# Optimization experiments

Measured on AMD Instinct MI355X. Metric: run time of the kernel, lower is better.

Reference implementation:

```python
import jax, jax.numpy as jnp
import numpy as np

B, T, D, H, FA = 512, 64, 128, 128, 64


def setup_inputs() -> dict:
    key = jax.random.key(0)
    ks = jax.random.split(key, 14)
    n = lambda k, s: jax.random.normal(k, s, dtype=jnp.float32) * 0.05
    return {
        "X": jax.random.normal(ks[0], (B, T, D), dtype=jnp.float32),
        "attri_data": jax.random.normal(ks[1], (D, FA), dtype=jnp.float32),
        "w_attr1": n(ks[2], (FA, FA // 2)), "b_attr1": n(ks[3], (FA // 2,)),
        "w_attr2": n(ks[4], (FA // 2, 1)), "b_attr2": n(ks[5], (1,)),
        "w_a1": n(ks[6], (2 * H + T, H)), "b_a1": n(ks[7], (H,)),
        "w_a2": n(ks[8], (H, 1)), "b_a2": n(ks[9], (1,)),
        "w_ih": n(ks[10], (4 * H, D)), "w_hh": n(ks[11], (4 * H, H)),
        "b_ih": n(ks[12], (4 * H,)), "b_hh": n(ks[13], (4 * H,)),
    }


def reference(X, attri_data, w_attr1, b_attr1, w_attr2, b_attr2,
              w_a1, b_a1, w_a2, b_a2, w_ih, w_hh, b_ih, b_hh):
    b, t_dim, d = X.shape
    h_dim = w_hh.shape[1]

    # Attribute attention: softmax over the data_dim axis (dim=0)
    a = attri_data @ w_attr1 + b_attr1
    a = jnp.where(a > 0, a, 0.5 * a)  # LeakyReLU(negative_slope=0.5)
    alpha_attri = jax.nn.softmax(a @ w_attr2 + b_attr2, axis=0)  # [D, 1]
    X_attri = X * alpha_attri.reshape(1, 1, d)  # [B, T, D]
    Xp = jnp.transpose(X_attri, (0, 2, 1))      # [B, D, T] per-variable series

    def step(carry, x_t):  # x_t: [B, D]
        h, c = carry  # [B, H] each; state BEFORE consuming x_t (matches torch loop)
        feat = jnp.concatenate([
            jnp.broadcast_to(h[:, None, :], (b, d, h_dim)),
            jnp.broadcast_to(c[:, None, :], (b, d, h_dim)),
            Xp,
        ], axis=2)  # [B, D, 2H+T]
        e = jnp.tanh(feat @ w_a1 + b_a1) @ w_a2 + b_a2  # [B, D, 1]
        alpha_s = jax.nn.softmax(e[..., 0], axis=1)      # softmax over D
        x_tilde_t = alpha_s * x_t                        # [B, D]
        # LSTM cell (PyTorch gate order i, f, g, o)
        gates = x_t @ w_ih.T + b_ih + h @ w_hh.T + b_hh  # [B, 4H]
        i_g, f_g, g_g, o_g = jnp.split(gates, 4, axis=1)
        c_new = jax.nn.sigmoid(f_g) * c + jax.nn.sigmoid(i_g) * jnp.tanh(g_g)
        h_new = jax.nn.sigmoid(o_g) * jnp.tanh(c_new)
        return (h_new, c_new), x_tilde_t

    h0 = jnp.zeros((b, h_dim), X.dtype)
    c0 = jnp.zeros((b, h_dim), X.dtype)
    _, X_tilde = jax.lax.scan(step, (h0, c0), jnp.transpose(X_attri, (1, 0, 2)))
    return jnp.transpose(X_tilde, (1, 0, 2))  # [B, T, D]
```

## Files before the change

### kernel.cpp

```cpp
#include <hip/hip_runtime.h>
#include <hip/hip_bf16.h>
#include <cstddef>
#include <cstdint>

#define DEVI __device__ __forceinline__

typedef float f32x4 __attribute__((ext_vector_type(4)));
typedef __bf16 bf16x8 __attribute__((ext_vector_type(8)));

DEVI float fast_rcp(float x) { return __builtin_amdgcn_rcpf(x); }
DEVI float sigmoid_fast(float x) { return fast_rcp(1.0f + __expf(-x)); }
DEVI float tanh_fast(float x) { return 1.0f - 2.0f * fast_rcp(__expf(2.0f * x) + 1.0f); }
DEVI float4 ld4(const float* p) { return *reinterpret_cast<const float4*>(p); }
DEVI void st4(float* p, float4 v) { *reinterpret_cast<float4*>(p) = v; }
DEVI float f4c(const float4& v, int i) { return i == 0 ? v.x : i == 1 ? v.y : i == 2 ? v.z : v.w; }
DEVI unsigned short bfbits(float f) { return __builtin_bit_cast(unsigned short, (__bf16)f); }
DEVI unsigned pack2(float a, float b) {
  return (unsigned)bfbits(a) | ((unsigned)bfbits(b) << 16);
}

__global__ __launch_bounds__(128) void k_alpha(
    const float* __restrict__ AD, const float* __restrict__ W1,
    const float* __restrict__ B1, const float* __restrict__ W2,
    const float* __restrict__ B2, float* __restrict__ alpha) {
  __shared__ float sW1[64 * 32];
  __shared__ float sW2[32];
  __shared__ float sB1[32];
  __shared__ float red[128];
  __shared__ float s_mx, s_sum;
  int tid = threadIdx.x;
  for (int i = tid; i < 64 * 32; i += 128) sW1[i] = W1[i];
  if (tid < 32) { sW2[tid] = W2[tid]; sB1[tid] = B1[tid]; }
  __syncthreads();
  float ad[64];
  #pragma unroll
  for (int f = 0; f < 64; ++f) ad[f] = AD[tid * 64 + f];
  float logit = B2[0];
  #pragma unroll
  for (int j = 0; j < 32; ++j) {
    float a = sB1[j];
    #pragma unroll
    for (int f = 0; f < 64; ++f) a = fmaf(ad[f], sW1[f * 32 + j], a);
    a = a > 0.0f ? a : 0.5f * a;
    logit = fmaf(a, sW2[j], logit);
  }
  red[tid] = logit;
  __syncthreads();
  if (tid == 0) {
    float mx = red[0];
    for (int i = 1; i < 128; ++i) mx = fmaxf(mx, red[i]);
    float sm = 0.0f;
    for (int i = 0; i < 128; ++i) sm += __expf(red[i] - mx);
    s_mx = mx; s_sum = sm;
  }
  __syncthreads();
  alpha[tid] = __expf(logit - s_mx) / s_sum;
}

__global__ __launch_bounds__(256) void k_ep(
    const float* __restrict__ X, const float* __restrict__ w_a1,
    const float* __restrict__ b_a1, const float* __restrict__ alpha,
    float* __restrict__ EP) {
  __shared__ float Xb[64][128];
  __shared__ float Wx[64][128];
  int b = blockIdx.x;
  int tid = threadIdx.x;
  #pragma unroll
  for (int i = 0; i < 8; ++i) {
    int l4 = i * 256 + tid;
    int r = l4 >> 5, c4 = l4 & 31;
    st4(&Xb[r][c4 * 4], ld4(&X[((size_t)b * 64 + r) * 128 + c4 * 4]));
    st4(&Wx[r][c4 * 4], ld4(&w_a1[(size_t)(256 + r) * 128 + c4 * 4]));
  }
  __syncthreads();
  int dg = tid & 15, kg = tid >> 4;
  float acc[8][8] = {};
  #pragma unroll 4
  for (int tau = 0; tau < 64; ++tau) {
    float4 xa0 = ld4(&Xb[tau][dg * 4]);
    float4 xa1 = ld4(&Xb[tau][64 + dg * 4]);
    float4 wa0 = ld4(&Wx[tau][kg * 4]);
    float4 wa1 = ld4(&Wx[tau][64 + kg * 4]);
    #pragma unroll
    for (int i = 0; i < 8; ++i) {
      float xv = (i < 4) ? f4c(xa0, i) : f4c(xa1, i - 4);
      #pragma unroll
      for (int j = 0; j < 4; ++j) {
        acc[i][j]     = fmaf(xv, f4c(wa0, j), acc[i][j]);
        acc[i][j + 4] = fmaf(xv, f4c(wa1, j), acc[i][j + 4]);
      }
    }
  }
  float4 ba0 = ld4(&b_a1[kg * 4]);
  float4 ba1v = ld4(&b_a1[64 + kg * 4]);
  #pragma unroll
  for (int i = 0; i < 8; ++i) {
    int drow = (i < 4) ? dg * 4 + i : 64 + dg * 4 + (i - 4);
    float al = alpha[drow];
    float4 o0, o1;
    float* p0 = &o0.x; float* p1 = &o1.x;
    #pragma unroll
    for (int j = 0; j < 4; ++j) {
      float v0 = 2.0f * fmaf(al, acc[i][j],     f4c(ba0, j));
      float v1 = 2.0f * fmaf(al, acc[i][j + 4], f4c(ba1v, j));
      p0[j] = __expf(fminf(fmaxf(v0, -40.0f), 40.0f));
      p1[j] = __expf(fminf(fmaxf(v1, -40.0f), 40.0f));
    }
    st4(&EP[((size_t)b * 128 + drow) * 128 + kg * 4], o0);
    st4(&EP[((size_t)b * 128 + drow) * 128 + 64 + kg * 4], o1);
  }
}

__global__ __launch_bounds__(512, 2) void k_rec(
    const float* __restrict__ X, const float* __restrict__ w_ih,
    const float* __restrict__ w_hh, const float* __restrict__ b_ih,
    const float* __restrict__ b_hh, const float* __restrict__ alpha,
    float* __restrict__ S) {
  __shared__ unsigned short kB[16 * 256];
  int tid = threadIdx.x;
  int wv = tid >> 6, l = tid & 63, lg = l >> 4, lr = l & 15;
  int b0 = blockIdx.x * 16;

  bf16x8 afr[8][4];
  #pragma unroll
  for (int ks = 0; ks < 8; ++ks) {
    int kb = (ks & 3) * 32 + lg * 8;
    float4 a0, a1;
    if (ks < 4) { a0 = ld4(&alpha[kb]); a1 = ld4(&alpha[kb + 4]); }
    #pragma unroll
    for (int q = 0; q < 4; ++q) {
      int j = q * 128 + wv * 16 + lr;
      const float* src = (ks < 4) ? &w_ih[(size_t)j * 128 + kb]
                                  : &w_hh[(size_t)j * 128 + kb];
      float4 f0 = ld4(src), f1 = ld4(src + 4);
      if (ks < 4) {
        f0.x *= a0.x; f0.y *= a0.y; f0.z *= a0.z; f0.w *= a0.w;
        f1.x *= a1.x; f1.y *= a1.y; f1.z *= a1.z; f1.w *= a1.w;
      }
      bf16x8 fr;
      fr[0] = (__bf16)f0.x; fr[1] = (__bf16)f0.y;
      fr[2] = (__bf16)f0.z; fr[3] = (__bf16)f0.w;
      fr[4] = (__bf16)f1.x; fr[5] = (__bf16)f1.y;
      fr[6] = (__bf16)f1.z; fr[7] = (__bf16)f1.w;
      afr[ks][q] = fr;
    }
  }

  float bias[4][4];
  #pragma unroll
  for (int q = 0; q < 4; ++q)
    #pragma unroll
    for (int r = 0; r < 4; ++r) {
      int j = q * 128 + wv * 16 + lg * 4 + r;
      bias[q][r] = b_ih[j] + b_hh[j];
    }

  alignas(16) float hA[4] = {0.f, 0.f, 0.f, 0.f};
  alignas(16) float cA[4] = {0.f, 0.f, 0.f, 0.f};

  int bi = tid >> 5, d4 = tid & 31, d0 = d4 * 4;
  int m0 = wv * 16 + lg * 4;
  int k0 = 128 + m0;
  unsigned short* xdst = &kB[bi * 256 + (((d0 >> 3) ^ (bi & 7)) << 3) + (d0 & 7)];
  unsigned short* hdst = &kB[lr * 256 + ((((k0 >> 3) ^ (lr & 7))) << 3) + (k0 & 7)];

  for (int t = 0; t < 64; ++t) {
    size_t srow = ((size_t)(t * 512) + b0 + lr) * 256;
    st4(&S[srow + m0], *reinterpret_cast<const float4*>(hA));
    st4(&S[srow + 128 + m0], *reinterpret_cast<const float4*>(cA));

    float4 xv = ld4(&X[(((size_t)(b0 + bi)) * 64 + t) * 128 + d0]);
    uint2 xu; xu.x = pack2(xv.x, xv.y); xu.y = pack2(xv.z, xv.w);
    *reinterpret_cast<uint2*>(xdst) = xu;

    uint2 hu; hu.x = pack2(hA[0], hA[1]); hu.y = pack2(hA[2], hA[3]);
    *reinterpret_cast<uint2*>(hdst) = hu;

    __syncthreads();

    bf16x8 bfr[8];
    #pragma unroll
    for (int ks = 0; ks < 8; ++ks) {
      int kb = ks * 32 + lg * 8;
      int idx = lr * 256 + (((kb >> 3) ^ (lr & 7)) << 3) + (kb & 7);
      bfr[ks] = *reinterpret_cast<const bf16x8*>(&kB[idx]);
    }

    f32x4 acc0 = {0.f, 0.f, 0.f, 0.f}, acc1 = acc0, acc2 = acc0, acc3 = acc0;
    #pragma unroll
    for (int ks = 0; ks < 8; ++ks) {
      acc0 = __builtin_amdgcn_mfma_f32_16x16x32_bf16(afr[ks][0], bfr[ks], acc0, 0, 0, 0);
      acc1 = __builtin_amdgcn_mfma_f32_16x16x32_bf16(afr[ks][1], bfr[ks], acc1, 0, 0, 0);
      acc2 = __builtin_amdgcn_mfma_f32_16x16x32_bf16(afr[ks][2], bfr[ks], acc2, 0, 0, 0);
      acc3 = __builtin_amdgcn_mfma_f32_16x16x32_bf16(afr[ks][3], bfr[ks], acc3, 0, 0, 0);
    }

    #pragma unroll
    for (int r = 0; r < 4; ++r) {
      float ig = sigmoid_fast(acc0[r] + bias[0][r]);
      float fg = sigmoid_fast(acc1[r] + bias[1][r]);
      float gg = tanh_fast(acc2[r] + bias[2][r]);
      float og = sigmoid_fast(acc3[r] + bias[3][r]);
      float cn = fmaf(fg, cA[r], ig * gg);
      float hn = og * tanh_fast(cn);
      cA[r] = cn;
      hA[r] = hn;
    }
    __syncthreads();
  }
}

__global__ __launch_bounds__(256) void k_eq(
    const float* __restrict__ S, const float* __restrict__ w_a1,
    float* __restrict__ EQ) {
  __shared__ float Ss[64][68];
  __shared__ float Wc[64][128];
  int r0 = blockIdx.x * 64;
  int tid = threadIdx.x;
  int kg = tid & 15, rg = tid >> 4;
  int rr = rg * 4;
  float acc[4][8] = {};
  for (int kc = 0; kc < 4; ++kc) {
    if (kc) __syncthreads();
    #pragma unroll
    for (int i = 0; i < 4; ++i) {
      int l4 = i * 256 + tid;
      int r = l4 >> 4, c4 = l4 & 15;
      st4(&Ss[r][c4 * 4], ld4(&S[(size_t)(r0 + r) * 256 + kc * 64 + c4 * 4]));
    }
    #pragma unroll
    for (int i = 0; i < 8; ++i) {
      int l4 = i * 256 + tid;
      int r = l4 >> 5, c4 = l4 & 31;
      st4(&Wc[r][c4 * 4], ld4(&w_a1[(size_t)(kc * 64 + r) * 128 + c4 * 4]));
    }
    __syncthreads();
    #pragma unroll 2
    for (int k = 0; k < 64; k += 4) {
      float4 sa[4];
      #pragma unroll
      for (int i = 0; i < 4; ++i) sa[i] = ld4(&Ss[rr + i][k]);
      #pragma unroll
      for (int kk = 0; kk < 4; ++kk) {
        float4 wa0 = ld4(&Wc[k + kk][kg * 4]);
        float4 wa1 = ld4(&Wc[k + kk][64 + kg * 4]);
        #pragma unroll
        for (int i = 0; i < 4; ++i) {
          float sv = f4c(sa[i], kk);
          #pragma unroll
          for (int j = 0; j < 4; ++j) {
            acc[i][j]     = fmaf(sv, f4c(wa0, j), acc[i][j]);
            acc[i][j + 4] = fmaf(sv, f4c(wa1, j), acc[i][j + 4]);
          }
        }
      }
    }
  }
  #pragma unroll
  for (int i = 0; i < 4; ++i) {
    float4 o0, o1;
    float* p0 = &o0.x; float* p1 = &o1.x;
    #pragma unroll
    for (int j = 0; j < 4; ++j) {
      float v0 = 2.0f * acc[i][j];
      float v1 = 2.0f * acc[i][j + 4];
      p0[j] = __expf(fminf(fmaxf(v0, -40.0f), 40.0f));
      p1[j] = __expf(fminf(fmaxf(v1, -40.0f), 40.0f));
    }
    st4(&EQ[(size_t)(r0 + rr + i) * 128 + kg * 4], o0);
    st4(&EQ[(size_t)(r0 + rr + i) * 128 + 64 + kg * 4], o1);
  }
}

__global__ __launch_bounds__(512, 4) void k_attn(
    const float* __restrict__ EP, const float* __restrict__ EQ,
    const float* __restrict__ w_a2, const float* __restrict__ alpha,
    const float* __restrict__ X, float* __restrict__ out) {
  __shared__ float EQs[64][128];
  __shared__ float e_lds[128];
  int b = blockIdx.x;
  int tid = threadIdx.x;
  #pragma unroll
  for (int i = 0; i < 4; ++i) {
    int l4 = i * 512 + tid;
    int t = l4 >> 5, k4 = l4 & 31;
    st4(&EQs[t][k4 * 4], ld4(&EQ[((size_t)t * 512 + b) * 128 + k4 * 4]));
  }
  int d = tid >> 2, s = tid & 3;
  float4 ep[8], w2r[8];
  #pragma unroll
  for (int q = 0; q < 8; ++q) {
    ep[q]  = ld4(&EP[((size_t)b * 128 + d) * 128 + s * 32 + q * 4]);
    w2r[q] = ld4(&w_a2[s * 32 + q * 4]);
  }
  __syncthreads();
  for (int t = 0; t < 64; ++t) {
    float p = 0.0f;
    #pragma unroll
    for (int q = 0; q < 8; ++q) {
      float4 eq = ld4(&EQs[t][s * 32 + q * 4]);
      p = fmaf(w2r[q].x, fast_rcp(fmaf(ep[q].x, eq.x, 1.0f)), p);
      p = fmaf(w2r[q].y, fast_rcp(fmaf(ep[q].y, eq.y, 1.0f)), p);
      p = fmaf(w2r[q].z, fast_rcp(fmaf(ep[q].z, eq.z, 1.0f)), p);
      p = fmaf(w2r[q].w, fast_rcp(fmaf(ep[q].w, eq.w, 1.0f)), p);
    }
    p += __shfl_xor(p, 1);
    p += __shfl_xor(p, 2);
    if (s == 0) e_lds[d] = -2.0f * p;
    __syncthreads();
    if (tid < 128) {
      int lane = tid & 63;
      float v0 = e_lds[lane], v1 = e_lds[64 + lane];
      float mx = fmaxf(v0, v1);
      #pragma unroll
      for (int o = 1; o < 64; o <<= 1) mx = fmaxf(mx, __shfl_xor(mx, o));
      float e0 = __expf(v0 - mx), e1 = __expf(v1 - mx);
      float sm = e0 + e1;
      #pragma unroll
      for (int o = 1; o < 64; o <<= 1) sm += __shfl_xor(sm, o);
      float inv = fast_rcp(sm);
      float ev = (tid < 64) ? e0 : e1;
      float av = ev * inv * alpha[tid];
      out[((size_t)b * 64 + t) * 128 + tid] = av * X[((size_t)b * 64 + t) * 128 + tid];
    }
    __syncthreads();
  }
}

extern "C" void kernel_launch(void* const* d_in, const int* in_sizes, int n_in,
                              void* d_out, int out_size, void* d_ws, size_t ws_size,
                              hipStream_t stream) {
  const float* X    = (const float*)d_in[0];
  const float* AD   = (const float*)d_in[1];
  const float* W1   = (const float*)d_in[2];
  const float* B1   = (const float*)d_in[3];
  const float* W2   = (const float*)d_in[4];
  const float* B2   = (const float*)d_in[5];
  const float* w_a1 = (const float*)d_in[6];
  const float* b_a1 = (const float*)d_in[7];
  const float* w_a2 = (const float*)d_in[8];
  const float* w_ih = (const float*)d_in[10];
  const float* w_hh = (const float*)d_in[11];
  const float* b_ih = (const float*)d_in[12];
  const float* b_hh = (const float*)d_in[13];
  float* out = (float*)d_out;
  float* ws = (float*)d_ws;

  float* alpha = ws;
  float* EQ    = ws + 256;
  float* EP    = EQ + 4194304;
  float* S     = EP + 8388608;

  hipLaunchKernelGGL(k_alpha, dim3(1), dim3(128), 0, stream, AD, W1, B1, W2, B2, alpha);
  hipLaunchKernelGGL(k_ep,   dim3(512), dim3(256), 0, stream, X, w_a1, b_a1, alpha, EP);
  hipLaunchKernelGGL(k_rec,  dim3(32),  dim3(512), 0, stream, X, w_ih, w_hh, b_ih, b_hh, alpha, S);
  hipLaunchKernelGGL(k_eq,   dim3(512), dim3(256), 0, stream, S, w_a1, EQ);
  hipLaunchKernelGGL(k_attn, dim3(512), dim3(512), 0, stream, EP, EQ, w_a2, alpha, X, out);
}
```

Baseline: 356.2 us.

## Double-buffer LSTM recurrence, store state in bf16, MFMA state projection, batch softmax rows

The recurrent kernel now double-buffers its LDS operand tile so each step needs one barrier instead of two. It also prefetches X rows three steps ahead and splits the x and h MFMA chains to shorten dependency latency. The saved h/c state is written as bf16, and the state-to-attention projection is rewritten as a bf16 MFMA GEMM against a pre-transposed bf16 copy of w_a1 produced by a new small kernel. The attention kernel now computes 8 timesteps per barrier round and runs the softmax on all 8 waves in parallel. The cost is lower precision in the h/c projection and one extra kernel launch.

```diff
diff --git a/kernel.cpp b/kernel.cpp
--- a/kernel.cpp
+++ b/kernel.cpp
@@ -57,6 +57,28 @@
   alpha[tid] = __expf(logit - s_mx) / s_sum;
 }
 
+__global__ __launch_bounds__(256) void k_tw(
+    const float* __restrict__ w_a1, __hip_bfloat16* __restrict__ w1T) {
+  __shared__ float tile[64][132];
+  int blk = blockIdx.x;
+  int tid = threadIdx.x;
+  #pragma unroll
+  for (int i = 0; i < 32; ++i) {
+    int idx = i * 256 + tid;
+    int r = idx >> 7, c = idx & 127;
+    tile[r][c] = w_a1[(size_t)(blk * 64 + r) * 128 + c];
+  }
+  __syncthreads();
+  int n = tid >> 1, mh = tid & 1;
+  unsigned* dst = reinterpret_cast<unsigned*>(&w1T[(size_t)n * 256 + blk * 64 + mh * 32]);
+  #pragma unroll
+  for (int i = 0; i < 16; ++i) {
+    float a = tile[mh * 32 + 2 * i][n];
+    float b = tile[mh * 32 + 2 * i + 1][n];
+    dst[i] = pack2(a, b);
+  }
+}
+
 __global__ __launch_bounds__(256) void k_ep(
     const float* __restrict__ X, const float* __restrict__ w_a1,
     const float* __restrict__ b_a1, const float* __restrict__ alpha,
@@ -111,12 +133,12 @@
   }
 }
 
-__global__ __launch_bounds__(512, 2) void k_rec(
+__global__ __launch_bounds__(512, 1) void k_rec(
     const float* __restrict__ X, const float* __restrict__ w_ih,
     const float* __restrict__ w_hh, const float* __restrict__ b_ih,
     const float* __restrict__ b_hh, const float* __restrict__ alpha,
-    float* __restrict__ S) {
-  __shared__ unsigned short kB[16 * 256];
+    __hip_bfloat16* __restrict__ S) {
+  __shared__ unsigned short kB[2][16 * 256];
   int tid = threadIdx.x;
   int wv = tid >> 6, l = tid & 63, lg = l >> 4, lr = l & 15;
   int b0 = blockIdx.x * 16;
@@ -158,126 +180,138 @@
   alignas(16) float hA[4] = {0.f, 0.f, 0.f, 0.f};
   alignas(16) float cA[4] = {0.f, 0.f, 0.f, 0.f};
 
-  int bi = tid >> 5, d4 = tid & 31, d0 = d4 * 4;
+  int bi = tid >> 5, d0 = (tid & 31) * 4;
   int m0 = wv * 16 + lg * 4;
   int k0 = 128 + m0;
-  unsigned short* xdst = &kB[bi * 256 + (((d0 >> 3) ^ (bi & 7)) << 3) + (d0 & 7)];
-  unsigned short* hdst = &kB[lr * 256 + ((((k0 >> 3) ^ (lr & 7))) << 3) + (k0 & 7)];
+  int xoff = bi * 256 + (((d0 >> 3) ^ (bi & 7)) << 3) + (d0 & 7);
+  int hoff = lr * 256 + (((k0 >> 3) ^ (lr & 7)) << 3) + (k0 & 7);
+
+  const float* xbase = &X[(size_t)(b0 + bi) * 64 * 128 + d0];
+
+  {
+    float4 x0 = ld4(xbase);
+    uint2 xu; xu.x = pack2(x0.x, x0.y); xu.y = pack2(x0.z, x0.w);
+    *reinterpret_cast<uint2*>(&kB[0][xoff]) = xu;
+    uint2 z; z.x = 0u; z.y = 0u;
+    *reinterpret_cast<uint2*>(&kB[0][hoff]) = z;
+  }
+  float4 xa = ld4(xbase + 1 * 128);
+  float4 xb = ld4(xbase + 2 * 128);
+  __syncthreads();
 
   for (int t = 0; t < 64; ++t) {
-    size_t srow = ((size_t)(t * 512) + b0 + lr) * 256;
-    st4(&S[srow + m0], *reinterpret_cast<const float4*>(hA));
-    st4(&S[srow + 128 + m0], *reinterpret_cast<const float4*>(cA));
-
-    float4 xv = ld4(&X[(((size_t)(b0 + bi)) * 64 + t) * 128 + d0]);
-    uint2 xu; xu.x = pack2(xv.x, xv.y); xu.y = pack2(xv.z, xv.w);
-    *reinterpret_cast<uint2*>(xdst) = xu;
-
-    uint2 hu; hu.x = pack2(hA[0], hA[1]); hu.y = pack2(hA[2], hA[3]);
-    *reinterpret_cast<uint2*>(hdst) = hu;
-
-    __syncthreads();
+    int cur = t & 1, nxt = cur ^ 1;
 
     bf16x8 bfr[8];
     #pragma unroll
     for (int ks = 0; ks < 8; ++ks) {
       int kb = ks * 32 + lg * 8;
       int idx = lr * 256 + (((kb >> 3) ^ (lr & 7)) << 3) + (kb & 7);
-      bfr[ks] = *reinterpret_cast<const bf16x8*>(&kB[idx]);
-    }
-
-    f32x4 acc0 = {0.f, 0.f, 0.f, 0.f}, acc1 = acc0, acc2 = acc0, acc3 = acc0;
-    #pragma unroll
-    for (int ks = 0; ks < 8; ++ks) {
-      acc0 = __builtin_amdgcn_mfma_f32_16x16x32_bf16(afr[ks][0], bfr[ks], acc0, 0, 0, 0);
-      acc1 = __builtin_amdgcn_mfma_f32_16x16x32_bf16(afr[ks][1], bfr[ks], acc1, 0, 0, 0);
-      acc2 = __builtin_amdgcn_mfma_f32_16x16x32_bf16(afr[ks][2], bfr[ks], acc2, 0, 0, 0);
-      acc3 = __builtin_amdgcn_mfma_f32_16x16x32_bf16(afr[ks][3], bfr[ks], acc3, 0, 0, 0);
+      bfr[ks] = *reinterpret_cast<const bf16x8*>(&kB[cur][idx]);
+    }
+
+    int tn = (t + 3 < 64) ? t + 3 : 63;
+    float4 xc = ld4(xbase + (size_t)tn * 128);
+
+    size_t srow = ((size_t)(t * 512) + b0 + lr) * 256;
+    uint2 hS; hS.x = pack2(hA[0], hA[1]); hS.y = pack2(hA[2], hA[3]);
+    uint2 cS; cS.x = pack2(cA[0], cA[1]); cS.y = pack2(cA[2], cA[3]);
+    *reinterpret_cast<uint2*>(&S[srow + m0]) = hS;
+    *reinterpret_cast<uint2*>(&S[srow + 128 + m0]) = cS;
+
+    f32x4 aX[4], aH[4];
+    #pragma unroll
+    for (int q = 0; q < 4; ++q) { aX[q] = (f32x4){0.f,0.f,0.f,0.f}; aH[q] = (f32x4){0.f,0.f,0.f,0.f}; }
+    #pragma unroll
+    for (int ks = 0; ks < 4; ++ks) {
+      #pragma unroll
+      for (int q = 0; q < 4; ++q)
+        aX[q] = __builtin_amdgcn_mfma_f32_16x16x32_bf16(afr[ks][q], bfr[ks], aX[q], 0, 0, 0);
+      #pragma unroll
+      for (int q = 0; q < 4; ++q)
+        aH[q] = __builtin_amdgcn_mfma_f32_16x16x32_bf16(afr[ks + 4][q], bfr[ks + 4], aH[q], 0, 0, 0);
     }
 
     #pragma unroll
     for (int r = 0; r < 4; ++r) {
-      float ig = sigmoid_fast(acc0[r] + bias[0][r]);
-      float fg = sigmoid_fast(acc1[r] + bias[1][r]);
-      float gg = tanh_fast(acc2[r] + bias[2][r]);
-      float og = sigmoid_fast(acc3[r] + bias[3][r]);
+      float g0 = aX[0][r] + aH[0][r] + bias[0][r];
+      float g1 = aX[1][r] + aH[1][r] + bias[1][r];
+      float g2 = aX[2][r] + aH[2][r] + bias[2][r];
+      float g3 = aX[3][r] + aH[3][r] + bias[3][r];
+      float ig = sigmoid_fast(g0);
+      float fg = sigmoid_fast(g1);
+      float gg = tanh_fast(g2);
+      float og = sigmoid_fast(g3);
       float cn = fmaf(fg, cA[r], ig * gg);
       float hn = og * tanh_fast(cn);
       cA[r] = cn;
       hA[r] = hn;
     }
+
+    uint2 xu; xu.x = pack2(xa.x, xa.y); xu.y = pack2(xa.z, xa.w);
+    *reinterpret_cast<uint2*>(&kB[nxt][xoff]) = xu;
+    uint2 hu; hu.x = pack2(hA[0], hA[1]); hu.y = pack2(hA[2], hA[3]);
+    *reinterpret_cast<uint2*>(&kB[nxt][hoff]) = hu;
+    xa = xb; xb = xc;
     __syncthreads();
   }
 }
 
-__global__ __launch_bounds__(256) void k_eq(
-    const float* __restrict__ S, const float* __restrict__ w_a1,
+__global__ __launch_bounds__(256, 1) void k_eq(
+    const __hip_bfloat16* __restrict__ S, const __hip_bfloat16* __restrict__ w1T,
     float* __restrict__ EQ) {
-  __shared__ float Ss[64][68];
-  __shared__ float Wc[64][128];
-  int r0 = blockIdx.x * 64;
-  int tid = threadIdx.x;
-  int kg = tid & 15, rg = tid >> 4;
-  int rr = rg * 4;
-  float acc[4][8] = {};
-  for (int kc = 0; kc < 4; ++kc) {
-    if (kc) __syncthreads();
-    #pragma unroll
-    for (int i = 0; i < 4; ++i) {
-      int l4 = i * 256 + tid;
-      int r = l4 >> 4, c4 = l4 & 15;
-      st4(&Ss[r][c4 * 4], ld4(&S[(size_t)(r0 + r) * 256 + kc * 64 + c4 * 4]));
-    }
-    #pragma unroll
-    for (int i = 0; i < 8; ++i) {
-      int l4 = i * 256 + tid;
-      int r = l4 >> 5, c4 = l4 & 31;
-      st4(&Wc[r][c4 * 4], ld4(&w_a1[(size_t)(kc * 64 + r) * 128 + c4 * 4]));
-    }
-    __syncthreads();
-    #pragma unroll 2
-    for (int k = 0; k < 64; k += 4) {
-      float4 sa[4];
-      #pragma unroll
-      for (int i = 0; i < 4; ++i) sa[i] = ld4(&Ss[rr + i][k]);
-      #pragma unroll
-      for (int kk = 0; kk < 4; ++kk) {
-        float4 wa0 = ld4(&Wc[k + kk][kg * 4]);
-        float4 wa1 = ld4(&Wc[k + kk][64 + kg * 4]);
-        #pragma unroll
-        for (int i = 0; i < 4; ++i) {
-          float sv = f4c(sa[i], kk);
-          #pragma unroll
-          for (int j = 0; j < 4; ++j) {
-            acc[i][j]     = fmaf(sv, f4c(wa0, j), acc[i][j]);
-            acc[i][j + 4] = fmaf(sv, f4c(wa1, j), acc[i][j + 4]);
-          }
-        }
+  int tid = threadIdx.x;
+  int wv = tid >> 6, l = tid & 63;
+  int lr = l & 15, lg = l >> 4;
+  int r0 = blockIdx.x * 128 + wv * 32;
+
+  bf16x8 a[2][8];
+  #pragma unroll
+  for (int ri = 0; ri < 2; ++ri)
+    #pragma unroll
+    for (int ks = 0; ks < 8; ++ks)
+      a[ri][ks] = *reinterpret_cast<const bf16x8*>(
+          &S[(size_t)(r0 + ri * 16 + lr) * 256 + ks * 32 + lg * 8]);
+
+  f32x4 acc[2][8];
+  #pragma unroll
+  for (int ri = 0; ri < 2; ++ri)
+    #pragma unroll
+    for (int nj = 0; nj < 8; ++nj) acc[ri][nj] = (f32x4){0.f, 0.f, 0.f, 0.f};
+
+  #pragma unroll
+  for (int nj = 0; nj < 8; ++nj) {
+    bf16x8 bf[8];
+    #pragma unroll
+    for (int ks = 0; ks < 8; ++ks)
+      bf[ks] = *reinterpret_cast<const bf16x8*>(
+          &w1T[(size_t)(nj * 16 + lr) * 256 + ks * 32 + lg * 8]);
+    #pragma unroll
+    for (int ks = 0; ks < 8; ++ks) {
+      acc[0][nj] = __builtin_amdgcn_mfma_f32_16x16x32_bf16(a[0][ks], bf[ks], acc[0][nj], 0, 0, 0);
+      acc[1][nj] = __builtin_amdgcn_mfma_f32_16x16x32_bf16(a[1][ks], bf[ks], acc[1][nj], 0, 0, 0);
+    }
+  }
+
+  #pragma unroll
+  for (int ri = 0; ri < 2; ++ri)
+    #pragma unroll
+    for (int nj = 0; nj < 8; ++nj)
+      #pragma unroll
+      for (int r = 0; r < 4; ++r) {
+        int grow = r0 + ri * 16 + lg * 4 + r;
+        int n = nj * 16 + lr;
+        float v = 2.0f * acc[ri][nj][r];
+        EQ[(size_t)grow * 128 + n] = __expf(fminf(fmaxf(v, -40.f), 40.f));
       }
-    }
-  }
-  #pragma unroll
-  for (int i = 0; i < 4; ++i) {
-    float4 o0, o1;
-    float* p0 = &o0.x; float* p1 = &o1.x;
-    #pragma unroll
-    for (int j = 0; j < 4; ++j) {
-      float v0 = 2.0f * acc[i][j];
-      float v1 = 2.0f * acc[i][j + 4];
-      p0[j] = __expf(fminf(fmaxf(v0, -40.0f), 40.0f));
-      p1[j] = __expf(fminf(fmaxf(v1, -40.0f), 40.0f));
-    }
-    st4(&EQ[(size_t)(r0 + rr + i) * 128 + kg * 4], o0);
-    st4(&EQ[(size_t)(r0 + rr + i) * 128 + 64 + kg * 4], o1);
-  }
-}
-
-__global__ __launch_bounds__(512, 4) void k_attn(
+}
+
+__global__ __launch_bounds__(512, 2) void k_attn(
     const float* __restrict__ EP, const float* __restrict__ EQ,
     const float* __restrict__ w_a2, const float* __restrict__ alpha,
     const float* __restrict__ X, float* __restrict__ out) {
   __shared__ float EQs[64][128];
-  __shared__ float e_lds[128];
+  __shared__ float e_lds[8][128];
   int b = blockIdx.x;
   int tid = threadIdx.x;
   #pragma unroll
@@ -293,24 +327,31 @@
     ep[q]  = ld4(&EP[((size_t)b * 128 + d) * 128 + s * 32 + q * 4]);
     w2r[q] = ld4(&w_a2[s * 32 + q * 4]);
   }
-  __syncthreads();
-  for (int t = 0; t < 64; ++t) {
-    float p = 0.0f;
-    #pragma unroll
-    for (int q = 0; q < 8; ++q) {
-      float4 eq = ld4(&EQs[t][s * 32 + q * 4]);
-      p = fmaf(w2r[q].x, fast_rcp(fmaf(ep[q].x, eq.x, 1.0f)), p);
-      p = fmaf(w2r[q].y, fast_rcp(fmaf(ep[q].y, eq.y, 1.0f)), p);
-      p = fmaf(w2r[q].z, fast_rcp(fmaf(ep[q].z, eq.z, 1.0f)), p);
-      p = fmaf(w2r[q].w, fast_rcp(fmaf(ep[q].w, eq.w, 1.0f)), p);
-    }
-    p += __shfl_xor(p, 1);
-    p += __shfl_xor(p, 2);
-    if (s == 0) e_lds[d] = -2.0f * p;
+  int wv = tid >> 6, l = tid & 63;
+  float al0 = alpha[l], al1 = alpha[64 + l];
+  __syncthreads();
+
+  for (int rnd = 0; rnd < 8; ++rnd) {
+    #pragma unroll
+    for (int it = 0; it < 8; ++it) {
+      int t = rnd * 8 + it;
+      float p = 0.0f;
+      #pragma unroll
+      for (int q = 0; q < 8; ++q) {
+        float4 eq = ld4(&EQs[t][s * 32 + q * 4]);
+        p = fmaf(w2r[q].x, fast_rcp(fmaf(ep[q].x, eq.x, 1.0f)), p);
+        p = fmaf(w2r[q].y, fast_rcp(fmaf(ep[q].y, eq.y, 1.0f)), p);
+        p = fmaf(w2r[q].z, fast_rcp(fmaf(ep[q].z, eq.z, 1.0f)), p);
+        p = fmaf(w2r[q].w, fast_rcp(fmaf(ep[q].w, eq.w, 1.0f)), p);
+      }
+      p += __shfl_xor(p, 1);
+      p += __shfl_xor(p, 2);
+      if (s == 0) e_lds[it][d] = -2.0f * p;
+    }
     __syncthreads();
-    if (tid < 128) {
-      int lane = tid & 63;
-      float v0 = e_lds[lane], v1 = e_lds[64 + lane];
+    {
+      int t = rnd * 8 + wv;
+      float v0 = e_lds[wv][l], v1 = e_lds[wv][64 + l];
       float mx = fmaxf(v0, v1);
       #pragma unroll
       for (int o = 1; o < 64; o <<= 1) mx = fmaxf(mx, __shfl_xor(mx, o));
@@ -319,9 +360,9 @@
       #pragma unroll
       for (int o = 1; o < 64; o <<= 1) sm += __shfl_xor(sm, o);
       float inv = fast_rcp(sm);
-      float ev = (tid < 64) ? e0 : e1;
-      float av = ev * inv * alpha[tid];
-      out[((size_t)b * 64 + t) * 128 + tid] = av * X[((size_t)b * 64 + t) * 128 + tid];
+      size_t ro = ((size_t)b * 64 + t) * 128;
+      out[ro + l]      = e0 * inv * al0 * X[ro + l];
+      out[ro + 64 + l] = e1 * inv * al1 * X[ro + 64 + l];
     }
     __syncthreads();
   }
@@ -349,11 +390,13 @@
   float* alpha = ws;
   float* EQ    = ws + 256;
   float* EP    = EQ + 4194304;
-  float* S     = EP + 8388608;
-
-  hipLaunchKernelGGL(k_alpha, dim3(1), dim3(128), 0, stream, AD, W1, B1, W2, B2, alpha);
-  hipLaunchKernelGGL(k_ep,   dim3(512), dim3(256), 0, stream, X, w_a1, b_a1, alpha, EP);
-  hipLaunchKernelGGL(k_rec,  dim3(32),  dim3(512), 0, stream, X, w_ih, w_hh, b_ih, b_hh, alpha, S);
-  hipLaunchKernelGGL(k_eq,   dim3(512), dim3(256), 0, stream, S, w_a1, EQ);
-  hipLaunchKernelGGL(k_attn, dim3(512), dim3(512), 0, stream, EP, EQ, w_a2, alpha, X, out);
-}
+  __hip_bfloat16* S   = (__hip_bfloat16*)(EP + 8388608);
+  __hip_bfloat16* w1T = (__hip_bfloat16*)(EP + 8388608 + 4194304);
+
+  hipLaunchKernelGGL(k_alpha, dim3(1),   dim3(128), 0, stream, AD, W1, B1, W2, B2, alpha);
+  hipLaunchKernelGGL(k_tw,    dim3(4),   dim3(256), 0, stream, w_a1, w1T);
+  hipLaunchKernelGGL(k_ep,    dim3(512), dim3(256), 0, stream, X, w_a1, b_a1, alpha, EP);
+  hipLaunchKernelGGL(k_rec,   dim3(32),  dim3(512), 0, stream, X, w_ih, w_hh, b_ih, b_hh, alpha, S);
+  hipLaunchKernelGGL(k_eq,    dim3(256), dim3(256), 0, stream, S, w1T, EQ);
+  hipLaunchKernelGGL(k_attn,  dim3(512), dim3(512), 0, stream, EP, EQ, w_a2, alpha, X, out);
+}
```

Result: faster. 305.9 us (-14.1%).
